# Performance work log

Measured on AMD Instinct MI355X. Metric: run time of the kernel, lower is better.

Reference implementation:

```python
import jax, jax.numpy as jnp
import numpy as np

B, CIN, COUT, COFF = 1, 16, 32, 16
D, H, W = 32, 128, 160
K = 3
EPS = 1e-5  # torch BatchNorm default


def conv2d(x, w):
    return jax.lax.conv_general_dilated(x, w, (1, 1), [(1, 1), (1, 1)],
                                        dimension_numbers=('NCHW', 'OIHW', 'NCHW'))


def conv3d(x, w):
    return jax.lax.conv_general_dilated(x, w, (1, 1, 1), [(1, 1), (1, 1), (1, 1)],
                                        dimension_numbers=('NCDHW', 'OIDHW', 'NCDHW'))


def bn(x, gamma, beta, axes):
    # training-mode batch norm (batch statistics), matching torch BN in train mode
    m = jnp.mean(x, axis=axes, keepdims=True)
    v = jnp.var(x, axis=axes, keepdims=True)
    sh = [1] * x.ndim
    sh[1] = -1
    return (x - m) * jax.lax.rsqrt(v + EPS) * gamma.reshape(sh) + beta.reshape(sh)


def bilinear_gather(x, py, px):
    # x: [B,C,H,W]; py,px: [B,K2,H,W] float sample coords -> [B,C,K2,H,W]
    Bq, C, Hh, Ww = x.shape
    y0 = jnp.floor(py)
    x0 = jnp.floor(px)
    wy1 = py - y0
    wx1 = px - x0

    def g(yi, xi):
        yic = jnp.clip(yi, 0, Hh - 1).astype(jnp.int32)
        xic = jnp.clip(xi, 0, Ww - 1).astype(jnp.int32)
        mask = ((yi >= 0) & (yi <= Hh - 1) & (xi >= 0) & (xi <= Ww - 1)).astype(x.dtype)
        v = jax.vmap(lambda xb, yb, xc: xb[:, yb, xc])(x, yic, xic)  # [B,C,K2,H,W]
        return v * mask[:, None]

    return (g(y0, x0) * ((1.0 - wy1) * (1.0 - wx1))[:, None]
            + g(y0, x0 + 1.0) * ((1.0 - wy1) * wx1)[:, None]
            + g(y0 + 1.0, x0) * (wy1 * (1.0 - wx1))[:, None]
            + g(y0 + 1.0, x0 + 1.0) * (wy1 * wx1)[:, None])


def gd_slice(xs, ds, w_off, w_reg, g1, b1):
    # DeformableConv2dBnReLU on one depth slice: xs [B,CIN,H,W], ds [B,COFF,H,W]
    offset = jnp.clip(conv2d(ds, w_off), -1.0, 1.0)     # [B, 2*K*K, H, W]
    Bq = offset.shape[0]
    off = offset.reshape(Bq, K * K, 2, H, W)            # torchvision layout: (dy, dx) per tap
    ii = jnp.repeat(jnp.arange(K), K).astype(xs.dtype)  # kernel row index per tap
    jj = jnp.tile(jnp.arange(K), K).astype(xs.dtype)    # kernel col index per tap
    # base sampling grid (stride=1, pad=1, dilation=1) plus learned offsets
    py = (jnp.arange(H, dtype=xs.dtype)[None, :, None] - 1.0 + ii[:, None, None])[None] + off[:, :, 0]
    px = (jnp.arange(W, dtype=xs.dtype)[None, None, :] - 1.0 + jj[:, None, None])[None] + off[:, :, 1]
    sampled = bilinear_gather(xs, py, px)               # [B,CIN,K2,H,W]
    out = jnp.einsum('bckhw,ock->bohw', sampled, w_reg.reshape(COUT, CIN, K * K))
    return jax.nn.relu(bn(out, g1, b1, (0, 2, 3)))      # per-slice BN2d stats, as in the torch loop


def setup_inputs() -> dict:
    key = jax.random.key(0)
    ks = jax.random.split(key, 6)
    r = lambda k, sh, s=1.0: jax.random.normal(k, sh, dtype=jnp.float32) * s
    return {
        'x': r(ks[0], (B, CIN, D, H, W)),
        'f': r(ks[1], (B, COFF, D, H, W)),
        'w_off': r(ks[2], (2 * K * K, COFF, 3, 3), 0.05),
        'w_reg': r(ks[3], (COUT, CIN, K, K), 0.1),
        'g1': jnp.ones((COUT,), jnp.float32),
        'b1': jnp.zeros((COUT,), jnp.float32),
        'w2': r(ks[4], (COUT, COUT, K, K, K), 0.05),
        'g2': jnp.ones((COUT,), jnp.float32),
        'b2': jnp.zeros((COUT,), jnp.float32),
        'wd': r(ks[5], (COUT, CIN, K, K, K), 0.05),
        'gd': jnp.ones((COUT,), jnp.float32),
        'bd': jnp.zeros((COUT,), jnp.float32),
    }


def reference(x, f, w_off, w_reg, g1, b1, w2, g2, b2, wd, gd, bd):
    # GDConv3D: per-depth-slice deformable conv + BN2d + ReLU, vmapped over D
    out = jax.vmap(gd_slice, in_axes=(2, 2, None, None, None, None), out_axes=2)(
        x, f, w_off, w_reg, g1, b1)                      # [B,COUT,D,H,W]
    out = bn(conv3d(out, w2), g2, b2, (0, 2, 3, 4))
    identity = bn(conv3d(x, wd), gd, bd, (0, 2, 3, 4))   # downsample (CIN != COUT)
    return jax.nn.relu(out + identity)
```

## Files before the change

kernel.cpp:

```cpp
#include <hip/hip_runtime.h>

using u16 = unsigned short;

constexpr int CIN = 16, COUT = 32, COFF = 16;
constexpr int D = 32, H = 128, W = 160;
constexpr int HW = H * W;
constexpr int DHW = D * HW;
constexpr int NOUT = COUT * DHW;
constexpr float EPS = 1e-5f;

constexpr size_t WF_OFF = 16384;
constexpr size_t A1CH_OFF = 262144;
constexpr size_t XCH16_OFF = 42205184;
constexpr size_t FRAG2P_W2 = 84148224;
constexpr size_t FRAG2P_WD = 84203520;
constexpr size_t NEED_2PASS = 84258816;
constexpr size_t STA_OFF = 63176704;
constexpr size_t STB_OFF = 147062784;
constexpr size_t FRAGS_W2 = 230948864;
constexpr size_t FRAGS_WD = 231004160;
constexpr size_t NEED_STORE = 231059456;
constexpr int WOFF_O = 0, WREG_O = 2592, W2_O = 7200, WD_O = 34848;
constexpr int G1_O = 48672, B1_O = 48704, G2_O = 48736, B2_O = 48768, GD_O = 48800, BD_O = 48832;
constexpr int WOFFT_O = 49152, WREGT_O = 52224;
constexpr int FLAG_SLOT = 3000;

typedef short bf16x8 __attribute__((ext_vector_type(8)));
typedef float f32x4 __attribute__((ext_vector_type(4)));

static __device__ __forceinline__ float bf2f(u16 h) {
  unsigned u = ((unsigned)h) << 16;
  float f;
  __builtin_memcpy(&f, &u, 4);
  return f;
}
static __device__ __forceinline__ u16 f2bf(float f) {
  unsigned u;
  __builtin_memcpy(&u, &f, 4);
  u += 0x7fffu + ((u >> 16) & 1u);
  return (u16)(u >> 16);
}
static __device__ __forceinline__ float ldin(const void* p, int i, int bf) {
  float r;
  if (bf) r = bf2f(((const u16*)p)[i]);
  else r = ((const float*)p)[i];
  return r;
}

__global__ __launch_bounds__(256) void zero_kernel(float* __restrict__ S) {
  S[blockIdx.x * 256 + threadIdx.x] = 0.f;
}

__global__ __launch_bounds__(256) void sniff_kernel(const u16* __restrict__ x,
                                                    int* __restrict__ flag) {
  __shared__ int sh[256];
  int cnt = 0;
  for (int i = threadIdx.x; i < 4096; i += 256) {
    int e = (x[i] >> 7) & 0xff;
    cnt += (e >= 96 && e <= 144) ? 1 : 0;
  }
  sh[threadIdx.x] = cnt;
  __syncthreads();
  for (int s = 128; s > 0; s >>= 1) {
    if (threadIdx.x < (unsigned)s) sh[threadIdx.x] += sh[threadIdx.x + s];
    __syncthreads();
  }
  if (threadIdx.x == 0) flag[0] = (sh[0] > 3072) ? 1 : 0;
}

__global__ __launch_bounds__(256) void cvt_kernel(const void* __restrict__ in,
                                                  float* __restrict__ out, int n,
                                                  const int* __restrict__ flagp) {
  int bf = flagp[0];
  int i = blockIdx.x * 256 + threadIdx.x;
  if (i < n) out[i] = ldin(in, i, bf);
}

__global__ __launch_bounds__(256) void woff_t_kernel(const float* __restrict__ src,
                                                     float* __restrict__ dst) {
  int t = blockIdx.x * 256 + threadIdx.x;
  if (t >= 2592) return;
  int ch = t / 144, widx = t % 144;
  dst[widx * 18 + ch] = src[t];
}

__global__ __launch_bounds__(256) void wreg_t_kernel(const float* __restrict__ src,
                                                     float* __restrict__ dst) {
  int t = blockIdx.x * 256 + threadIdx.x;
  if (t >= 4608) return;
  int co = t / 144, k = t % 144;
  dst[k * 32 + co] = src[t];
}

__global__ __launch_bounds__(256) void pack_frag_kernel(const float* __restrict__ src,
                                                        u16* __restrict__ dst, int nci) {
  int t = blockIdx.x * 256 + threadIdx.x;
  if (t >= 27648) return;
  int j = t & 7;
  int l = (t >> 3) & 63;
  int cotile = (t >> 9) & 1;
  int tap = t >> 10;
  int co = cotile * 16 + (l & 15);
  int k = (l >> 4) * 8 + j;
  float v = (k < nci) ? src[(co * nci + k) * 27 + tap] : 0.f;
  dst[t] = f2bf(v);
}

__global__ __launch_bounds__(256) void chpose_kernel(const void* __restrict__ src,
                                                     u16* __restrict__ dst,
                                                     const int* __restrict__ flagp) {
  const int bf = flagp[0];
  __shared__ u16 lt[16][258];
  const int base = blockIdx.x * 256;
  const int t = threadIdx.x;
#pragma unroll
  for (int ci = 0; ci < 16; ci++) lt[ci][t] = f2bf(ldin(src, ci * DHW + base + t, bf));
  __syncthreads();
  const size_t pb = (size_t)(base + t) * 16;
  uint4 u0, u1;
  u0.x = (unsigned)lt[0][t] | ((unsigned)lt[1][t] << 16);
  u0.y = (unsigned)lt[2][t] | ((unsigned)lt[3][t] << 16);
  u0.z = (unsigned)lt[4][t] | ((unsigned)lt[5][t] << 16);
  u0.w = (unsigned)lt[6][t] | ((unsigned)lt[7][t] << 16);
  u1.x = (unsigned)lt[8][t] | ((unsigned)lt[9][t] << 16);
  u1.y = (unsigned)lt[10][t] | ((unsigned)lt[11][t] << 16);
  u1.z = (unsigned)lt[12][t] | ((unsigned)lt[13][t] << 16);
  u1.w = (unsigned)lt[14][t] | ((unsigned)lt[15][t] << 16);
  *(uint4*)(dst + pb) = u0;
  *(uint4*)(dst + pb + 8) = u1;
}

__global__ __launch_bounds__(256) void deform_chm_kernel(const void* __restrict__ x,
                                                         const void* __restrict__ f,
                                                         const float* __restrict__ w_off_t,
                                                         const float* __restrict__ w_reg_t,
                                                         u16* __restrict__ a1ch,
                                                         const int* __restrict__ flagp,
                                                         float* __restrict__ S) {
  const int bf = flagp[0];
  const int hw = blockIdx.x;
  const int bid = (hw & 7) * 320 + (hw >> 3);
  const int d = bid / 80;
  const int p = (bid % 80) * 256 + threadIdx.x;
  const int y = p / W;
  const int xx = p % W;
  const int dbase = d * HW;

  float doff[18];
#pragma unroll
  for (int t = 0; t < 18; t++) doff[t] = 0.f;
  for (int ci = 0; ci < COFF; ci++) {
    const int fbase = ci * DHW + dbase;
#pragma unroll
    for (int ki = 0; ki < 3; ki++) {
      int yy = y - 1 + ki;
      bool yok = (unsigned)yy < (unsigned)H;
#pragma unroll
      for (int kj = 0; kj < 3; kj++) {
        int xj = xx - 1 + kj;
        float v = (yok && (unsigned)xj < (unsigned)W) ? ldin(f, fbase + yy * W + xj, bf) : 0.f;
        int widx = ci * 9 + ki * 3 + kj;
#pragma unroll
        for (int t = 0; t < 18; t++) doff[t] += v * w_off_t[widx * 18 + t];
      }
    }
  }

  float acc[COUT];
#pragma unroll
  for (int co = 0; co < COUT; co++) acc[co] = 0.f;

#pragma unroll
  for (int t = 0; t < 9; t++) {
    float dy = fminf(fmaxf(doff[2 * t], -1.f), 1.f);
    float dx = fminf(fmaxf(doff[2 * t + 1], -1.f), 1.f);
    float py = (float)(y - 1 + t / 3) + dy;
    float px = (float)(xx - 1 + t % 3) + dx;
    float y0f = floorf(py), x0f = floorf(px);
    float wy1 = py - y0f, wx1 = px - x0f;
    int y0 = (int)y0f, x0i = (int)x0f;
    int y1 = y0 + 1, x1 = x0i + 1;
    bool y0v = (unsigned)y0 < (unsigned)H, y1v = (unsigned)y1 < (unsigned)H;
    bool x0v = (unsigned)x0i < (unsigned)W, x1v = (unsigned)x1 < (unsigned)W;
    float c00 = (y0v && x0v) ? (1.f - wy1) * (1.f - wx1) : 0.f;
    float c01 = (y0v && x1v) ? (1.f - wy1) * wx1 : 0.f;
    float c10 = (y1v && x0v) ? wy1 * (1.f - wx1) : 0.f;
    float c11 = (y1v && x1v) ? wy1 * wx1 : 0.f;
    int y0c = min(max(y0, 0), H - 1) * W, y1c = min(max(y1, 0), H - 1) * W;
    int x0c = min(max(x0i, 0), W - 1), x1c = min(max(x1, 0), W - 1);

    for (int ci = 0; ci < CIN; ci++) {
      const int xbase = ci * DHW + dbase;
      float s = c00 * ldin(x, xbase + y0c + x0c, bf) + c01 * ldin(x, xbase + y0c + x1c, bf) +
                c10 * ldin(x, xbase + y1c + x0c, bf) + c11 * ldin(x, xbase + y1c + x1c, bf);
      const float* wp = w_reg_t + (ci * 9 + t) * 32;
#pragma unroll
      for (int co = 0; co < COUT; co++) acc[co] += s * wp[co];
    }
  }

  u16 hh[COUT];
#pragma unroll
  for (int co = 0; co < COUT; co++) hh[co] = f2bf(acc[co]);
  const size_t pb = ((size_t)dbase + p) * 32;
#pragma unroll
  for (int k = 0; k < 4; k++) {
    uint4 u;
    u.x = (unsigned)hh[8 * k + 0] | ((unsigned)hh[8 * k + 1] << 16);
    u.y = (unsigned)hh[8 * k + 2] | ((unsigned)hh[8 * k + 3] << 16);
    u.z = (unsigned)hh[8 * k + 4] | ((unsigned)hh[8 * k + 5] << 16);
    u.w = (unsigned)hh[8 * k + 6] | ((unsigned)hh[8 * k + 7] << 16);
    *(uint4*)(a1ch + pb + 8 * k) = u;
  }

  const int l = threadIdx.x & 63;
  const int wv = threadIdx.x >> 6;
  __shared__ float ls[128], lq[128];
#pragma unroll
  for (int co = 0; co < COUT; co++) {
    float v = bf2f(hh[co]);
    float s = v, qq = v * v;
    s += __shfl_xor(s, 1);  qq += __shfl_xor(qq, 1);
    s += __shfl_xor(s, 2);  qq += __shfl_xor(qq, 2);
    s += __shfl_xor(s, 4);  qq += __shfl_xor(qq, 4);
    s += __shfl_xor(s, 8);  qq += __shfl_xor(qq, 8);
    s += __shfl_xor(s, 16); qq += __shfl_xor(qq, 16);
    s += __shfl_xor(s, 32); qq += __shfl_xor(qq, 32);
    if (l == 0) { ls[wv * 32 + co] = s; lq[wv * 32 + co] = qq; }
  }
  __syncthreads();
  if (threadIdx.x < 32) {
    int c = threadIdx.x;
    float s = ls[c] + ls[32 + c] + ls[64 + c] + ls[96 + c];
    float qq = lq[c] + lq[32 + c] + lq[64 + c] + lq[96 + c];
    atomicAdd(&S[c * D + d], s);
    atomicAdd(&S[1024 + c * D + d], qq);
  }
}

__global__ __launch_bounds__(256) void bn1_scale_kernel(float* __restrict__ S,
                                                        const float* __restrict__ g1f,
                                                        const float* __restrict__ b1f) {
  int cd = blockIdx.x * 256 + threadIdx.x;
  if (cd >= 1024) return;
  int c = cd / D;
  float mean = S[cd] / (float)HW;
  float var = S[1024 + cd] / (float)HW - mean * mean;
  float sc = g1f[c] * rsqrtf(var + EPS);
  S[cd] = sc;
  S[1024 + cd] = b1f[c] - mean * sc;
}

__global__ __launch_bounds__(256) void bn1_apply_ch_kernel(u16* __restrict__ a1ch,
                                                           const float* __restrict__ S) {
  __shared__ float sc[32], of[32];
  const int b = blockIdx.x;
  const int d = b / (HW / 256);
  if (threadIdx.x < 32) {
    sc[threadIdx.x] = S[threadIdx.x * D + d];
    of[threadIdx.x] = S[1024 + threadIdx.x * D + d];
  }
  __syncthreads();
  const size_t pb = ((size_t)b * 256 + threadIdx.x) * 32;
#pragma unroll
  for (int k = 0; k < 4; k++) {
    uint4 u = *(const uint4*)(a1ch + pb + 8 * k);
    unsigned w[4] = {u.x, u.y, u.z, u.w};
    unsigned ov[4];
#pragma unroll
    for (int m = 0; m < 4; m++) {
      int c0 = k * 8 + m * 2;
      float lo = bf2f((u16)(w[m] & 0xffffu));
      float hi = bf2f((u16)(w[m] >> 16));
      lo = fmaxf(lo * sc[c0] + of[c0], 0.f);
      hi = fmaxf(hi * sc[c0 + 1] + of[c0 + 1], 0.f);
      ov[m] = (unsigned)f2bf(lo) | ((unsigned)f2bf(hi) << 16);
    }
    uint4 o;
    o.x = ov[0]; o.y = ov[1]; o.z = ov[2]; o.w = ov[3];
    *(uint4*)(a1ch + pb + 8 * k) = o;
  }
}

typedef u16 u16x8 __attribute__((ext_vector_type(8)));

static __device__ __forceinline__ void conv_core_lds(const bf16x8* __restrict__ a1v,
                                                     const bf16x8* __restrict__ xv16,
                                                     const bf16x8* __restrict__ w2s,
                                                     const bf16x8* __restrict__ wdv,
                                                     int d, int y, int xn, int q, int l,
                                                     f32x4& A0, f32x4& A1, f32x4& B0, f32x4& B1) {
  const bf16x8 zero = {0, 0, 0, 0, 0, 0, 0, 0};
  const bool qlo = (q < 2);
#pragma unroll
  for (int kd = 0; kd < 3; kd++) {
    int dd = d - 1 + kd;
    if ((unsigned)dd >= (unsigned)D) continue;
#pragma unroll
    for (int ky = 0; ky < 3; ky++) {
      int yy = y - 1 + ky;
      if ((unsigned)yy >= (unsigned)H) continue;
      const int rowb = dd * HW + yy * W;
#pragma unroll
      for (int kx = 0; kx < 3; kx++) {
        int xx = xn - 1 + kx;
        bool ok = (unsigned)xx < (unsigned)W;
        int xc = min(max(xx, 0), W - 1);
        int pi = rowb + xc;
        bf16x8 bm = a1v[pi * 4 + q];
        bf16x8 bx = qlo ? xv16[pi * 2 + q] : zero;
        if (!ok) { bm = zero; bx = zero; }
        const int tb = (kd * 9 + ky * 3 + kx) * 2;
        bf16x8 am0 = w2s[(tb + 0) * 64 + l];
        bf16x8 am1 = w2s[(tb + 1) * 64 + l];
        bf16x8 ad0 = qlo ? wdv[(tb + 0) * 64 + l] : zero;
        bf16x8 ad1 = qlo ? wdv[(tb + 1) * 64 + l] : zero;
        A0 = __builtin_amdgcn_mfma_f32_16x16x32_bf16(am0, bm, A0, 0, 0, 0);
        A1 = __builtin_amdgcn_mfma_f32_16x16x32_bf16(am1, bm, A1, 0, 0, 0);
        B0 = __builtin_amdgcn_mfma_f32_16x16x32_bf16(ad0, bx, B0, 0, 0, 0);
        B1 = __builtin_amdgcn_mfma_f32_16x16x32_bf16(ad1, bx, B1, 0, 0, 0);
      }
    }
  }
}

#define STATS_RED(ACC, BASE)                                                          \
  {                                                                                   \
    _Pragma("unroll") for (int r = 0; r < 4; r++) {                                   \
      float v = ACC[r];                                                               \
      float s = v, qq = v * v;                                                        \
      s += __shfl_xor(s, 1); qq += __shfl_xor(qq, 1);                                 \
      s += __shfl_xor(s, 2); qq += __shfl_xor(qq, 2);                                 \
      s += __shfl_xor(s, 4); qq += __shfl_xor(qq, 4);                                 \
      s += __shfl_xor(s, 8); qq += __shfl_xor(qq, 8);                                 \
      if (n == 0) {                                                                   \
        int ci = (BASE) + q * 4 + r;                                                  \
        ls[wv * 64 + ci] = s;                                                         \
        lq[wv * 64 + ci] = qq;                                                        \
      }                                                                               \
    }                                                                                 \
  }

#define STATS_RED2(Aa, Ab, BASE)                                                      \
  {                                                                                   \
    _Pragma("unroll") for (int r = 0; r < 4; r++) {                                   \
      float v0 = Aa[r], v1 = Ab[r];                                                   \
      float s = v0 + v1, qq = v0 * v0 + v1 * v1;                                      \
      s += __shfl_xor(s, 1); qq += __shfl_xor(qq, 1);                                 \
      s += __shfl_xor(s, 2); qq += __shfl_xor(qq, 2);                                 \
      s += __shfl_xor(s, 4); qq += __shfl_xor(qq, 4);                                 \
      s += __shfl_xor(s, 8); qq += __shfl_xor(qq, 8);                                 \
      if (n == 0) {                                                                   \
        int ci = (BASE) + q * 4 + r;                                                  \
        ls[wv * 64 + ci] = s;                                                         \
        lq[wv * 64 + ci] = qq;                                                        \
      }                                                                               \
    }                                                                                 \
  }

__global__ __launch_bounds__(1024) void conv_mfma_store_kernel(const u16* __restrict__ a1ch,
                                                               const u16* __restrict__ xch16,
                                                               const u16* __restrict__ w2f,
                                                               const u16* __restrict__ wdf,
                                                               float* __restrict__ A,
                                                               float* __restrict__ Bb,
                                                               float* __restrict__ S) {
  __shared__ u16 w2s[27648];
  __shared__ float ls[16 * 64], lq[16 * 64];
  {
    const uint4* src = (const uint4*)w2f;
    uint4* dst = (uint4*)w2s;
    for (int i = threadIdx.x; i < 3456; i += 1024) dst[i] = src[i];
  }
  __syncthreads();

  const int hw = blockIdx.x;
  const int bid = (hw & 7) * 160 + (hw >> 3);
  const int t = threadIdx.x;
  const int l = t & 63, wv = t >> 6;
  const int n = l & 15, q = l >> 4;
  const int P0 = bid * 512 + wv * 32;
  const int d = P0 / HW;
  const int rp0 = P0 % HW;
  const int y0 = rp0 / W, x0 = rp0 % W;
  const int rp1 = (P0 + 16) % HW;
  const int y1g = rp1 / W, x1g = rp1 % W;

  const bf16x8 zero = {0, 0, 0, 0, 0, 0, 0, 0};
  const bool qlo = (q < 2);
  const bf16x8* a1v = (const bf16x8*)a1ch;
  const bf16x8* xv16 = (const bf16x8*)xch16;
  const bf16x8* w2v = (const bf16x8*)w2s;
  const bf16x8* wdv = (const bf16x8*)wdf;

  f32x4 aA0[2], aA1[2], aB0[2], aB1[2];
#pragma unroll
  for (int g = 0; g < 2; g++) {
    aA0[g] = (f32x4){0.f, 0.f, 0.f, 0.f};
    aA1[g] = (f32x4){0.f, 0.f, 0.f, 0.f};
    aB0[g] = (f32x4){0.f, 0.f, 0.f, 0.f};
    aB1[g] = (f32x4){0.f, 0.f, 0.f, 0.f};
  }

#pragma unroll
  for (int kd = 0; kd < 3; kd++) {
    int dd = d - 1 + kd;
    if ((unsigned)dd >= (unsigned)D) continue;
#pragma unroll
    for (int ky = 0; ky < 3; ky++) {
      int yy0 = y0 - 1 + ky, yy1 = y1g - 1 + ky;
      bool yok0 = (unsigned)yy0 < (unsigned)H, yok1 = (unsigned)yy1 < (unsigned)H;
      int rb0 = dd * HW + min(max(yy0, 0), H - 1) * W;
      int rb1 = dd * HW + min(max(yy1, 0), H - 1) * W;
#pragma unroll
      for (int kx = 0; kx < 3; kx++) {
        const int tb = (kd * 9 + ky * 3 + kx) * 2;
        bf16x8 am0 = w2v[(tb + 0) * 64 + l];
        bf16x8 am1 = w2v[(tb + 1) * 64 + l];
        bf16x8 ad0 = qlo ? wdv[(tb + 0) * 64 + l] : zero;
        bf16x8 ad1 = qlo ? wdv[(tb + 1) * 64 + l] : zero;
        {
          int xx = x0 + n - 1 + kx;
          bool ok = yok0 && (unsigned)xx < (unsigned)W;
          int pi = rb0 + min(max(xx, 0), W - 1);
          bf16x8 bm = a1v[pi * 4 + q];
          bf16x8 bx = qlo ? xv16[pi * 2 + q] : zero;
          if (!ok) { bm = zero; bx = zero; }
          aA0[0] = __builtin_amdgcn_mfma_f32_16x16x32_bf16(am0, bm, aA0[0], 0, 0, 0);
          aA1[0] = __builtin_amdgcn_mfma_f32_16x16x32_bf16(am1, bm, aA1[0], 0, 0, 0);
          aB0[0] = __builtin_amdgcn_mfma_f32_16x16x32_bf16(ad0, bx, aB0[0], 0, 0, 0);
          aB1[0] = __builtin_amdgcn_mfma_f32_16x16x32_bf16(ad1, bx, aB1[0], 0, 0, 0);
        }
        {
          int xx = x1g + n - 1 + kx;
          bool ok = yok1 && (unsigned)xx < (unsigned)W;
          int pi = rb1 + min(max(xx, 0), W - 1);
          bf16x8 bm = a1v[pi * 4 + q];
          bf16x8 bx = qlo ? xv16[pi * 2 + q] : zero;
          if (!ok) { bm = zero; bx = zero; }
          aA0[1] = __builtin_amdgcn_mfma_f32_16x16x32_bf16(am0, bm, aA0[1], 0, 0, 0);
          aA1[1] = __builtin_amdgcn_mfma_f32_16x16x32_bf16(am1, bm, aA1[1], 0, 0, 0);
          aB0[1] = __builtin_amdgcn_mfma_f32_16x16x32_bf16(ad0, bx, aB0[1], 0, 0, 0);
          aB1[1] = __builtin_amdgcn_mfma_f32_16x16x32_bf16(ad1, bx, aB1[1], 0, 0, 0);
        }
      }
    }
  }

#pragma unroll
  for (int g = 0; g < 2; g++) {
    const int Pg = P0 + 16 * g;
#pragma unroll
    for (int r = 0; r < 4; r++) {
      int co = q * 4 + r;
      A[co * DHW + Pg + n] = aA0[g][r];
      A[(co + 16) * DHW + Pg + n] = aA1[g][r];
      Bb[co * DHW + Pg + n] = aB0[g][r];
      Bb[(co + 16) * DHW + Pg + n] = aB1[g][r];
    }
  }

  STATS_RED2(aA0[0], aA0[1], 0)
  STATS_RED2(aA1[0], aA1[1], 16)
  STATS_RED2(aB0[0], aB0[1], 32)
  STATS_RED2(aB1[0], aB1[1], 48)
  __syncthreads();
  if (t < 64) {
    float s = 0.f, qq = 0.f;
    for (int w = 0; w < 16; w++) { s += ls[w * 64 + t]; qq += lq[w * 64 + t]; }
    if (t < 32) {
      atomicAdd(&S[2048 + t], s);
      atomicAdd(&S[2080 + t], qq);
    } else {
      atomicAdd(&S[2112 + t - 32], s);
      atomicAdd(&S[2144 + t - 32], qq);
    }
  }
}

__global__ __launch_bounds__(1024) void conv_mfma_stats_kernel(const u16* __restrict__ a1ch,
                                                               const u16* __restrict__ xch16,
                                                               const u16* __restrict__ w2f,
                                                               const u16* __restrict__ wdf,
                                                               float* __restrict__ S) {
  __shared__ u16 w2s[27648];
  __shared__ float ls[16 * 64], lq[16 * 64];
  {
    const uint4* src = (const uint4*)w2f;
    uint4* dst = (uint4*)w2s;
    for (int i = threadIdx.x; i < 3456; i += 1024) dst[i] = src[i];
  }
  __syncthreads();

  const int hw = blockIdx.x;
  const int bid = (hw & 7) * 320 + (hw >> 3);
  const int t = threadIdx.x;
  const int l = t & 63, wv = t >> 6;
  const int n = l & 15, q = l >> 4;
  const int P = bid * 256 + wv * 16;
  const int d = P / HW;
  const int rp = P % HW;
  const int y = rp / W, xc0 = rp % W;

  f32x4 A0 = {0.f, 0.f, 0.f, 0.f}, A1 = {0.f, 0.f, 0.f, 0.f};
  f32x4 B0 = {0.f, 0.f, 0.f, 0.f}, B1 = {0.f, 0.f, 0.f, 0.f};
  conv_core_lds((const bf16x8*)a1ch, (const bf16x8*)xch16, (const bf16x8*)w2s,
                (const bf16x8*)wdf, d, y, xc0 + n, q, l, A0, A1, B0, B1);

  STATS_RED(A0, 0)
  STATS_RED(A1, 16)
  STATS_RED(B0, 32)
  STATS_RED(B1, 48)
  __syncthreads();
  if (t < 64) {
    float s = 0.f, qq = 0.f;
    for (int w = 0; w < 16; w++) { s += ls[w * 64 + t]; qq += lq[w * 64 + t]; }
    if (t < 32) {
      atomicAdd(&S[2048 + t], s);
      atomicAdd(&S[2080 + t], qq);
    } else {
      atomicAdd(&S[2112 + t - 32], s);
      atomicAdd(&S[2144 + t - 32], qq);
    }
  }
}

__global__ void bn3_final_kernel(float* __restrict__ S, const float* __restrict__ g2f,
                                 const float* __restrict__ b2f, const float* __restrict__ gdf,
                                 const float* __restrict__ bdf) {
  int t = threadIdx.x;
  if (t < 32) {
    float mean = S[2048 + t] / (float)DHW;
    float var = S[2080 + t] / (float)DHW - mean * mean;
    float sc = g2f[t] * rsqrtf(var + EPS);
    S[2176 + t] = sc;
    S[2208 + t] = b2f[t] - mean * sc;
  } else {
    int c = t - 32;
    float mean = S[2112 + c] / (float)DHW;
    float var = S[2144 + c] / (float)DHW - mean * mean;
    float sc = gdf[c] * rsqrtf(var + EPS);
    S[2240 + c] = sc;
    S[2272 + c] = bdf[c] - mean * sc;
  }
}

__global__ __launch_bounds__(256) void combine32_kernel(const float* __restrict__ A,
                                                        const float* __restrict__ Bb,
                                                        const float* __restrict__ S,
                                                        const int* __restrict__ flagp,
                                                        void* __restrict__ out) {
  int i = (blockIdx.x * 256 + threadIdx.x) * 4;
  int co = i / DHW;
  float s2 = S[2176 + co], o2 = S[2208 + co];
  float sd = S[2240 + co], od = S[2272 + co];
  float4 va = *(const float4*)(A + i);
  float4 vb = *(const float4*)(Bb + i);
  float r0 = fmaxf(va.x * s2 + o2 + vb.x * sd + od, 0.f);
  float r1 = fmaxf(va.y * s2 + o2 + vb.y * sd + od, 0.f);
  float r2 = fmaxf(va.z * s2 + o2 + vb.z * sd + od, 0.f);
  float r3 = fmaxf(va.w * s2 + o2 + vb.w * sd + od, 0.f);
  int bf = flagp[0];
  if (bf) {
    ushort4 st;
    st.x = f2bf(r0); st.y = f2bf(r1); st.z = f2bf(r2); st.w = f2bf(r3);
    *(ushort4*)((u16*)out + i) = st;
  } else {
    float4 st;
    st.x = r0; st.y = r1; st.z = r2; st.w = r3;
    *(float4*)((float*)out + i) = st;
  }
}

__global__ __launch_bounds__(256) void conv_mfma_final_kernel(const u16* __restrict__ a1ch,
                                                              const u16* __restrict__ xch16,
                                                              const u16* __restrict__ w2f,
                                                              const u16* __restrict__ wdf,
                                                              const float* __restrict__ S,
                                                              const int* __restrict__ flagp,
                                                              void* __restrict__ out) {
  __shared__ u16 w2s[27648];
  {
    const uint4* src = (const uint4*)w2f;
    uint4* dst = (uint4*)w2s;
    for (int i = threadIdx.x; i < 3456; i += 256) dst[i] = src[i];
  }
  __syncthreads();

  const int hw = blockIdx.x;
  const int bid = (hw & 7) * 1280 + (hw >> 3);
  const int t = threadIdx.x;
  const int l = t & 63, wv = t >> 6;
  const int n = l & 15, q = l >> 4;
  const int P = bid * 64 + wv * 16;
  const int d = P / HW;
  const int rp = P % HW;
  const int y = rp / W, xc0 = rp % W;

  f32x4 A0 = {0.f, 0.f, 0.f, 0.f}, A1 = {0.f, 0.f, 0.f, 0.f};
  f32x4 B0 = {0.f, 0.f, 0.f, 0.f}, B1 = {0.f, 0.f, 0.f, 0.f};
  conv_core_lds((const bf16x8*)a1ch, (const bf16x8*)xch16, (const bf16x8*)w2s,
                (const bf16x8*)wdf, d, y, xc0 + n, q, l, A0, A1, B0, B1);

  const int bf = flagp[0];
#pragma unroll
  for (int r = 0; r < 4; r++) {
    int co = q * 4 + r;
    {
      float s2 = S[2176 + co], o2 = S[2208 + co];
      float sd = S[2240 + co], od = S[2272 + co];
      float v = fmaxf(A0[r] * s2 + o2 + B0[r] * sd + od, 0.f);
      int ai = co * DHW + P + n;
      if (bf) ((u16*)out)[ai] = f2bf(v);
      else ((float*)out)[ai] = v;
    }
    {
      int c2 = co + 16;
      float s2 = S[2176 + c2], o2 = S[2208 + c2];
      float sd = S[2240 + c2], od = S[2272 + c2];
      float v = fmaxf(A1[r] * s2 + o2 + B1[r] * sd + od, 0.f);
      int ai = c2 * DHW + P + n;
      if (bf) ((u16*)out)[ai] = f2bf(v);
      else ((float*)out)[ai] = v;
    }
  }
}

extern "C" void kernel_launch(void* const* d_in, const int* in_sizes, int n_in,
                              void* d_out, int out_size, void* d_ws, size_t ws_size,
                              hipStream_t stream) {
  const void* x = d_in[0];
  const void* f = d_in[1];

  char* ws = (char*)d_ws;
  float* S = (float*)ws;
  int* flag = (int*)ws + FLAG_SLOT;
  float* WF = (float*)(ws + WF_OFF);
  u16* a1ch = (u16*)(ws + A1CH_OFF);
  u16* xch16 = (u16*)(ws + XCH16_OFF);

  zero_kernel<<<16, 256, 0, stream>>>(S);
  sniff_kernel<<<1, 256, 0, stream>>>((const u16*)x, flag);

  const int cvt_n[10] = {2592, 4608, 27648, 13824, 32, 32, 32, 32, 32, 32};
  const int cvt_off[10] = {WOFF_O, WREG_O, W2_O, WD_O, G1_O, B1_O, G2_O, B2_O, GD_O, BD_O};
  const int src_idx[10] = {2, 3, 6, 9, 4, 5, 7, 8, 10, 11};
  for (int k = 0; k < 10; k++) {
    cvt_kernel<<<(cvt_n[k] + 255) / 256, 256, 0, stream>>>(d_in[src_idx[k]], WF + cvt_off[k],
                                                           cvt_n[k], flag);
  }

  const int store = (ws_size >= NEED_STORE) ? 1 : 0;
  u16* w2frag = (u16*)(ws + (store ? FRAGS_W2 : FRAG2P_W2));
  u16* wdfrag = (u16*)(ws + (store ? FRAGS_WD : FRAG2P_WD));

  woff_t_kernel<<<11, 256, 0, stream>>>(WF + WOFF_O, WF + WOFFT_O);
  wreg_t_kernel<<<18, 256, 0, stream>>>(WF + WREG_O, WF + WREGT_O);
  pack_frag_kernel<<<108, 256, 0, stream>>>(WF + W2_O, w2frag, 32);
  pack_frag_kernel<<<108, 256, 0, stream>>>(WF + WD_O, wdfrag, 16);
  chpose_kernel<<<DHW / 256, 256, 0, stream>>>(x, xch16, flag);

  deform_chm_kernel<<<2560, 256, 0, stream>>>(x, f, WF + WOFFT_O, WF + WREGT_O, a1ch, flag, S);
  bn1_scale_kernel<<<4, 256, 0, stream>>>(S, WF + G1_O, WF + B1_O);
  bn1_apply_ch_kernel<<<DHW / 256, 256, 0, stream>>>(a1ch, S);

  if (store) {
    float* A = (float*)(ws + STA_OFF);
    float* Bb = (float*)(ws + STB_OFF);
    conv_mfma_store_kernel<<<1280, 1024, 0, stream>>>(a1ch, xch16, w2frag, wdfrag, A, Bb, S);
    bn3_final_kernel<<<1, 64, 0, stream>>>(S, WF + G2_O, WF + B2_O, WF + GD_O, WF + BD_O);
    combine32_kernel<<<NOUT / 1024, 256, 0, stream>>>(A, Bb, S, flag, d_out);
  } else {
    conv_mfma_stats_kernel<<<2560, 1024, 0, stream>>>(a1ch, xch16, w2frag, wdfrag, S);
    bn3_final_kernel<<<1, 64, 0, stream>>>(S, WF + G2_O, WF + B2_O, WF + GD_O, WF + BD_O);
    conv_mfma_final_kernel<<<10240, 256, 0, stream>>>(a1ch, xch16, w2frag, wdfrag, S, flag,
                                                      d_out);
  }
}
```

Baseline: 731.1 us.

## Compute deformable conv regular weights with MFMA and fuse weight-prep launches

The deformable conv's scalar FP32 accumulation over 32 output channels is replaced by staging bilinear-sampled bf16 values in LDS and running 16x16x32 bf16 MFMA against pre-packed weight fragments. BN1 statistics are now reduced from the MFMA output layout. The fourteen small conversion and packing launches are merged into two kernels. This cuts VALU work and launch overhead, but it adds LDS traffic and a bf16 rounding of the sampled inputs before the matmul.

Measured after the change: 800.4 us. 1.09x slower.

```diff
diff --git a/kernel.cpp b/kernel.cpp
--- a/kernel.cpp
+++ b/kernel.cpp
@@ -10,6 +10,7 @@
 constexpr float EPS = 1e-5f;
 
 constexpr size_t WF_OFF = 16384;
+constexpr size_t DFRAG_OFF = 243712;
 constexpr size_t A1CH_OFF = 262144;
 constexpr size_t XCH16_OFF = 42205184;
 constexpr size_t FRAG2P_W2 = 84148224;
@@ -22,11 +23,12 @@
 constexpr size_t NEED_STORE = 231059456;
 constexpr int WOFF_O = 0, WREG_O = 2592, W2_O = 7200, WD_O = 34848;
 constexpr int G1_O = 48672, B1_O = 48704, G2_O = 48736, B2_O = 48768, GD_O = 48800, BD_O = 48832;
-constexpr int WOFFT_O = 49152, WREGT_O = 52224;
+constexpr int WOFFT_O = 49152;
 constexpr int FLAG_SLOT = 3000;
 
 typedef short bf16x8 __attribute__((ext_vector_type(8)));
 typedef float f32x4 __attribute__((ext_vector_type(4)));
+typedef u16 u16x8 __attribute__((ext_vector_type(8)));
 
 static __device__ __forceinline__ float bf2f(u16 h) {
   unsigned u = ((unsigned)h) << 16;
@@ -68,42 +70,69 @@
   if (threadIdx.x == 0) flag[0] = (sh[0] > 3072) ? 1 : 0;
 }
 
-__global__ __launch_bounds__(256) void cvt_kernel(const void* __restrict__ in,
-                                                  float* __restrict__ out, int n,
-                                                  const int* __restrict__ flagp) {
-  int bf = flagp[0];
+__global__ __launch_bounds__(256) void cvt_all_kernel(
+    const void* s0, const void* s1, const void* s2, const void* s3, const void* s4,
+    const void* s5, const void* s6, const void* s7, const void* s8, const void* s9,
+    float* __restrict__ WF, const int* __restrict__ flagp) {
+  const int bf = flagp[0];
   int i = blockIdx.x * 256 + threadIdx.x;
-  if (i < n) out[i] = ldin(in, i, bf);
-}
-
-__global__ __launch_bounds__(256) void woff_t_kernel(const float* __restrict__ src,
-                                                     float* __restrict__ dst) {
-  int t = blockIdx.x * 256 + threadIdx.x;
-  if (t >= 2592) return;
-  int ch = t / 144, widx = t % 144;
-  dst[widx * 18 + ch] = src[t];
-}
-
-__global__ __launch_bounds__(256) void wreg_t_kernel(const float* __restrict__ src,
-                                                     float* __restrict__ dst) {
-  int t = blockIdx.x * 256 + threadIdx.x;
-  if (t >= 4608) return;
-  int co = t / 144, k = t % 144;
-  dst[k * 32 + co] = src[t];
-}
-
-__global__ __launch_bounds__(256) void pack_frag_kernel(const float* __restrict__ src,
-                                                        u16* __restrict__ dst, int nci) {
-  int t = blockIdx.x * 256 + threadIdx.x;
-  if (t >= 27648) return;
-  int j = t & 7;
-  int l = (t >> 3) & 63;
-  int cotile = (t >> 9) & 1;
-  int tap = t >> 10;
-  int co = cotile * 16 + (l & 15);
-  int k = (l >> 4) * 8 + j;
-  float v = (k < nci) ? src[(co * nci + k) * 27 + tap] : 0.f;
-  dst[t] = f2bf(v);
+  if (i < 2592) { WF[WOFF_O + i] = ldin(s0, i, bf); return; }
+  i -= 2592;
+  if (i < 4608) { WF[WREG_O + i] = ldin(s1, i, bf); return; }
+  i -= 4608;
+  if (i < 27648) { WF[W2_O + i] = ldin(s2, i, bf); return; }
+  i -= 27648;
+  if (i < 13824) { WF[WD_O + i] = ldin(s3, i, bf); return; }
+  i -= 13824;
+  if (i < 32) { WF[G1_O + i] = ldin(s4, i, bf); return; }
+  i -= 32;
+  if (i < 32) { WF[B1_O + i] = ldin(s5, i, bf); return; }
+  i -= 32;
+  if (i < 32) { WF[G2_O + i] = ldin(s6, i, bf); return; }
+  i -= 32;
+  if (i < 32) { WF[B2_O + i] = ldin(s7, i, bf); return; }
+  i -= 32;
+  if (i < 32) { WF[GD_O + i] = ldin(s8, i, bf); return; }
+  i -= 32;
+  if (i < 32) { WF[BD_O + i] = ldin(s9, i, bf); }
+}
+
+__global__ __launch_bounds__(256) void prep_kernel(const float* __restrict__ WF,
+                                                   float* __restrict__ wofft,
+                                                   u16* __restrict__ w2frag,
+                                                   u16* __restrict__ wdfrag,
+                                                   u16* __restrict__ dfrag) {
+  int i = blockIdx.x * 256 + threadIdx.x;
+  if (i < 2592) {
+    int ch = i / 144, widx = i % 144;
+    wofft[widx * 18 + ch] = WF[WOFF_O + i];
+    return;
+  }
+  i -= 2592;
+  if (i < 27648) {
+    int j = i & 7, l = (i >> 3) & 63, cotile = (i >> 9) & 1, tap = i >> 10;
+    int co = cotile * 16 + (l & 15);
+    int k = (l >> 4) * 8 + j;
+    w2frag[i] = f2bf(WF[W2_O + (co * 32 + k) * 27 + tap]);
+    return;
+  }
+  i -= 27648;
+  if (i < 27648) {
+    int j = i & 7, l = (i >> 3) & 63, cotile = (i >> 9) & 1, tap = i >> 10;
+    int co = cotile * 16 + (l & 15);
+    int k = (l >> 4) * 8 + j;
+    float v = (k < 16) ? WF[WD_O + (co * 16 + k) * 27 + tap] : 0.f;
+    wdfrag[i] = f2bf(v);
+    return;
+  }
+  i -= 27648;
+  if (i < 5120) {
+    int j = i & 7, l = (i >> 3) & 63, ct = (i >> 9) & 1, c = i >> 10;
+    int k = c * 32 + (l >> 4) * 8 + j;
+    int co = ct * 16 + (l & 15);
+    float v = (k < 144) ? WF[WREG_O + co * 144 + (k & 15) * 9 + (k >> 4)] : 0.f;
+    dfrag[i] = f2bf(v);
+  }
 }
 
 __global__ __launch_bounds__(256) void chpose_kernel(const void* __restrict__ src,
@@ -130,13 +159,15 @@
   *(uint4*)(dst + pb + 8) = u1;
 }
 
-__global__ __launch_bounds__(256) void deform_chm_kernel(const void* __restrict__ x,
-                                                         const void* __restrict__ f,
-                                                         const float* __restrict__ w_off_t,
-                                                         const float* __restrict__ w_reg_t,
-                                                         u16* __restrict__ a1ch,
-                                                         const int* __restrict__ flagp,
-                                                         float* __restrict__ S) {
+__global__ __launch_bounds__(256) void deform_mfma_kernel(const void* __restrict__ x,
+                                                          const void* __restrict__ f,
+                                                          const float* __restrict__ w_off_t,
+                                                          const u16* __restrict__ dfrag,
+                                                          u16* __restrict__ a1ch,
+                                                          const int* __restrict__ flagp,
+                                                          float* __restrict__ S) {
+  __shared__ u16 slds[256 * 40];
+  __shared__ float ls[128], lq[128];
   const int bf = flagp[0];
   const int hw = blockIdx.x;
   const int bid = (hw & 7) * 320 + (hw >> 3);
@@ -166,68 +197,110 @@
     }
   }
 
-  float acc[COUT];
-#pragma unroll
-  for (int co = 0; co < COUT; co++) acc[co] = 0.f;
-
-#pragma unroll
-  for (int t = 0; t < 9; t++) {
-    float dy = fminf(fmaxf(doff[2 * t], -1.f), 1.f);
-    float dx = fminf(fmaxf(doff[2 * t + 1], -1.f), 1.f);
-    float py = (float)(y - 1 + t / 3) + dy;
-    float px = (float)(xx - 1 + t % 3) + dx;
-    float y0f = floorf(py), x0f = floorf(px);
-    float wy1 = py - y0f, wx1 = px - x0f;
-    int y0 = (int)y0f, x0i = (int)x0f;
-    int y1 = y0 + 1, x1 = x0i + 1;
-    bool y0v = (unsigned)y0 < (unsigned)H, y1v = (unsigned)y1 < (unsigned)H;
-    bool x0v = (unsigned)x0i < (unsigned)W, x1v = (unsigned)x1 < (unsigned)W;
-    float c00 = (y0v && x0v) ? (1.f - wy1) * (1.f - wx1) : 0.f;
-    float c01 = (y0v && x1v) ? (1.f - wy1) * wx1 : 0.f;
-    float c10 = (y1v && x0v) ? wy1 * (1.f - wx1) : 0.f;
-    float c11 = (y1v && x1v) ? wy1 * wx1 : 0.f;
-    int y0c = min(max(y0, 0), H - 1) * W, y1c = min(max(y1, 0), H - 1) * W;
-    int x0c = min(max(x0i, 0), W - 1), x1c = min(max(x1, 0), W - 1);
-
-    for (int ci = 0; ci < CIN; ci++) {
-      const int xbase = ci * DHW + dbase;
-      float s = c00 * ldin(x, xbase + y0c + x0c, bf) + c01 * ldin(x, xbase + y0c + x1c, bf) +
-                c10 * ldin(x, xbase + y1c + x0c, bf) + c11 * ldin(x, xbase + y1c + x1c, bf);
-      const float* wp = w_reg_t + (ci * 9 + t) * 32;
-#pragma unroll
-      for (int co = 0; co < COUT; co++) acc[co] += s * wp[co];
-    }
-  }
-
-  u16 hh[COUT];
-#pragma unroll
-  for (int co = 0; co < COUT; co++) hh[co] = f2bf(acc[co]);
-  const size_t pb = ((size_t)dbase + p) * 32;
-#pragma unroll
-  for (int k = 0; k < 4; k++) {
-    uint4 u;
-    u.x = (unsigned)hh[8 * k + 0] | ((unsigned)hh[8 * k + 1] << 16);
-    u.y = (unsigned)hh[8 * k + 2] | ((unsigned)hh[8 * k + 3] << 16);
-    u.z = (unsigned)hh[8 * k + 4] | ((unsigned)hh[8 * k + 5] << 16);
-    u.w = (unsigned)hh[8 * k + 6] | ((unsigned)hh[8 * k + 7] << 16);
-    *(uint4*)(a1ch + pb + 8 * k) = u;
-  }
-
   const int l = threadIdx.x & 63;
   const int wv = threadIdx.x >> 6;
-  __shared__ float ls[128], lq[128];
-#pragma unroll
-  for (int co = 0; co < COUT; co++) {
-    float v = bf2f(hh[co]);
-    float s = v, qq = v * v;
-    s += __shfl_xor(s, 1);  qq += __shfl_xor(qq, 1);
-    s += __shfl_xor(s, 2);  qq += __shfl_xor(qq, 2);
-    s += __shfl_xor(s, 4);  qq += __shfl_xor(qq, 4);
-    s += __shfl_xor(s, 8);  qq += __shfl_xor(qq, 8);
-    s += __shfl_xor(s, 16); qq += __shfl_xor(qq, 16);
-    s += __shfl_xor(s, 32); qq += __shfl_xor(qq, 32);
-    if (l == 0) { ls[wv * 32 + co] = s; lq[wv * 32 + co] = qq; }
-  }
+  const int n = l & 15, q = l >> 4;
+  const bf16x8* dfv = (const bf16x8*)dfrag;
+
+  f32x4 acc[4][2];
+#pragma unroll
+  for (int g = 0; g < 4; g++) {
+    acc[g][0] = (f32x4){0.f, 0.f, 0.f, 0.f};
+    acc[g][1] = (f32x4){0.f, 0.f, 0.f, 0.f};
+  }
+
+#pragma unroll
+  for (int c = 0; c < 5; c++) {
+#pragma unroll
+    for (int hf = 0; hf < 2; hf++) {
+      const int t = 2 * c + hf;
+      uint4 w0, w1;
+      if (t < 9) {
+        float dy = fminf(fmaxf(doff[2 * t], -1.f), 1.f);
+        float dx = fminf(fmaxf(doff[2 * t + 1], -1.f), 1.f);
+        float py = (float)(y - 1 + t / 3) + dy;
+        float px = (float)(xx - 1 + t % 3) + dx;
+        float y0f = floorf(py), x0f = floorf(px);
+        float wy1 = py - y0f, wx1 = px - x0f;
+        int y0 = (int)y0f, x0i = (int)x0f;
+        int y1 = y0 + 1, x1 = x0i + 1;
+        bool y0v = (unsigned)y0 < (unsigned)H, y1v = (unsigned)y1 < (unsigned)H;
+        bool x0v = (unsigned)x0i < (unsigned)W, x1v = (unsigned)x1 < (unsigned)W;
+        float c00 = (y0v && x0v) ? (1.f - wy1) * (1.f - wx1) : 0.f;
+        float c01 = (y0v && x1v) ? (1.f - wy1) * wx1 : 0.f;
+        float c10 = (y1v && x0v) ? wy1 * (1.f - wx1) : 0.f;
+        float c11 = (y1v && x1v) ? wy1 * wx1 : 0.f;
+        int y0c = min(max(y0, 0), H - 1) * W, y1c = min(max(y1, 0), H - 1) * W;
+        int x0c = min(max(x0i, 0), W - 1), x1c = min(max(x1, 0), W - 1);
+
+        u16 sv[16];
+#pragma unroll
+        for (int ci = 0; ci < CIN; ci++) {
+          const int xbase = ci * DHW + dbase;
+          float s = c00 * ldin(x, xbase + y0c + x0c, bf) + c01 * ldin(x, xbase + y0c + x1c, bf) +
+                    c10 * ldin(x, xbase + y1c + x0c, bf) + c11 * ldin(x, xbase + y1c + x1c, bf);
+          sv[ci] = f2bf(s);
+        }
+        w0.x = (unsigned)sv[0] | ((unsigned)sv[1] << 16);
+        w0.y = (unsigned)sv[2] | ((unsigned)sv[3] << 16);
+        w0.z = (unsigned)sv[4] | ((unsigned)sv[5] << 16);
+        w0.w = (unsigned)sv[6] | ((unsigned)sv[7] << 16);
+        w1.x = (unsigned)sv[8] | ((unsigned)sv[9] << 16);
+        w1.y = (unsigned)sv[10] | ((unsigned)sv[11] << 16);
+        w1.z = (unsigned)sv[12] | ((unsigned)sv[13] << 16);
+        w1.w = (unsigned)sv[14] | ((unsigned)sv[15] << 16);
+      } else {
+        w0.x = w0.y = w0.z = w0.w = 0u;
+        w1 = w0;
+      }
+      char* wp = (char*)slds + threadIdx.x * 80 + hf * 32;
+      *(uint4*)wp = w0;
+      *(uint4*)(wp + 16) = w1;
+    }
+    bf16x8 a0 = dfv[(c * 2 + 0) * 64 + l];
+    bf16x8 a1f = dfv[(c * 2 + 1) * 64 + l];
+#pragma unroll
+    for (int g = 0; g < 4; g++) {
+      const bf16x8 b = *(const bf16x8*)((const char*)slds + (wv * 64 + g * 16 + n) * 80 + q * 16);
+      acc[g][0] = __builtin_amdgcn_mfma_f32_16x16x32_bf16(a0, b, acc[g][0], 0, 0, 0);
+      acc[g][1] = __builtin_amdgcn_mfma_f32_16x16x32_bf16(a1f, b, acc[g][1], 0, 0, 0);
+    }
+  }
+
+  u16 hh[4][2][4];
+#pragma unroll
+  for (int g = 0; g < 4; g++)
+#pragma unroll
+    for (int ct = 0; ct < 2; ct++) {
+#pragma unroll
+      for (int r = 0; r < 4; r++) hh[g][ct][r] = f2bf(acc[g][ct][r]);
+      ushort4 st;
+      st.x = hh[g][ct][0];
+      st.y = hh[g][ct][1];
+      st.z = hh[g][ct][2];
+      st.w = hh[g][ct][3];
+      const size_t P = (size_t)bid * 256 + wv * 64 + g * 16 + n;
+      *(ushort4*)(a1ch + P * 32 + ct * 16 + q * 4) = st;
+    }
+
+#pragma unroll
+  for (int ct = 0; ct < 2; ct++)
+#pragma unroll
+    for (int r = 0; r < 4; r++) {
+      float v0 = bf2f(hh[0][ct][r]), v1 = bf2f(hh[1][ct][r]);
+      float v2 = bf2f(hh[2][ct][r]), v3 = bf2f(hh[3][ct][r]);
+      float s = v0 + v1 + v2 + v3;
+      float qq = v0 * v0 + v1 * v1 + v2 * v2 + v3 * v3;
+      s += __shfl_xor(s, 1); qq += __shfl_xor(qq, 1);
+      s += __shfl_xor(s, 2); qq += __shfl_xor(qq, 2);
+      s += __shfl_xor(s, 4); qq += __shfl_xor(qq, 4);
+      s += __shfl_xor(s, 8); qq += __shfl_xor(qq, 8);
+      if (n == 0) {
+        int co = ct * 16 + q * 4 + r;
+        ls[wv * 32 + co] = s;
+        lq[wv * 32 + co] = qq;
+      }
+    }
   __syncthreads();
   if (threadIdx.x < 32) {
     int c = threadIdx.x;
@@ -281,8 +354,6 @@
     *(uint4*)(a1ch + pb + 8 * k) = o;
   }
 }
-
-typedef u16 u16x8 __attribute__((ext_vector_type(8)));
 
 static __device__ __forceinline__ void conv_core_lds(const bf16x8* __restrict__ a1v,
                                                      const bf16x8* __restrict__ xv16,
@@ -636,31 +707,24 @@
   float* S = (float*)ws;
   int* flag = (int*)ws + FLAG_SLOT;
   float* WF = (float*)(ws + WF_OFF);
+  u16* dfrag = (u16*)(ws + DFRAG_OFF);
   u16* a1ch = (u16*)(ws + A1CH_OFF);
   u16* xch16 = (u16*)(ws + XCH16_OFF);
 
   zero_kernel<<<16, 256, 0, stream>>>(S);
   sniff_kernel<<<1, 256, 0, stream>>>((const u16*)x, flag);
 
-  const int cvt_n[10] = {2592, 4608, 27648, 13824, 32, 32, 32, 32, 32, 32};
-  const int cvt_off[10] = {WOFF_O, WREG_O, W2_O, WD_O, G1_O, B1_O, G2_O, B2_O, GD_O, BD_O};
-  const int src_idx[10] = {2, 3, 6, 9, 4, 5, 7, 8, 10, 11};
-  for (int k = 0; k < 10; k++) {
-    cvt_kernel<<<(cvt_n[k] + 255) / 256, 256, 0, stream>>>(d_in[src_idx[k]], WF + cvt_off[k],
-                                                           cvt_n[k], flag);
-  }
+  cvt_all_kernel<<<191, 256, 0, stream>>>(d_in[2], d_in[3], d_in[6], d_in[9], d_in[4], d_in[5],
+                                          d_in[7], d_in[8], d_in[10], d_in[11], WF, flag);
 
   const int store = (ws_size >= NEED_STORE) ? 1 : 0;
   u16* w2frag = (u16*)(ws + (store ? FRAGS_W2 : FRAG2P_W2));
   u16* wdfrag = (u16*)(ws + (store ? FRAGS_WD : FRAG2P_WD));
 
-  woff_t_kernel<<<11, 256, 0, stream>>>(WF + WOFF_O, WF + WOFFT_O);
-  wreg_t_kernel<<<18, 256, 0, stream>>>(WF + WREG_O, WF + WREGT_O);
-  pack_frag_kernel<<<108, 256, 0, stream>>>(WF + W2_O, w2frag, 32);
-  pack_frag_kernel<<<108, 256, 0, stream>>>(WF + WD_O, wdfrag, 16);
+  prep_kernel<<<247, 256, 0, stream>>>(WF, WF + WOFFT_O, w2frag, wdfrag, dfrag);
   chpose_kernel<<<DHW / 256, 256, 0, stream>>>(x, xch16, flag);
 
-  deform_chm_kernel<<<2560, 256, 0, stream>>>(x, f, WF + WOFFT_O, WF + WREGT_O, a1ch, flag, S);
+  deform_mfma_kernel<<<2560, 256, 0, stream>>>(x, f, WF + WOFFT_O, dfrag, a1ch, flag, S);
   bn1_scale_kernel<<<4, 256, 0, stream>>>(S, WF + G1_O, WF + B1_O);
   bn1_apply_ch_kernel<<<DHW / 256, 256, 0, stream>>>(a1ch, S);
 
```
